# Optimization experiments

Hardware: AMD Instinct MI355X
Metric: run time of the kernel (lower is better)

The kernel has to match this reference:

```python
import jax, jax.numpy as jnp
import numpy as np
from jax import lax

B, C_IN, H, W = 4, 1536, 24, 24
MID, DIM = 768, 384
HEADS = 8; DIM_HEAD = 48; GROUPS = 8
DS = 3; OFF_SCALE = 4.0; OFF_K = 3
CPB_DIM = DIM // 4  # 96


def conv1x1(x, w):
    # x: (B,Cin,H,W), w: (Cout,Cin)
    return jnp.einsum('bchw,oc->bohw', x, w)


def grouped_conv1x1(x, w):
    # x: (B,G*Ci,H,W), w: (G,Co,Ci)  == torch Conv2d(groups=G, k=1, bias=False)
    b, c, h, ww = x.shape
    g, co, ci = w.shape
    return jnp.einsum('bgihw,goi->bgohw', x.reshape(b, g, ci, h, ww), w).reshape(b, g * co, h, ww)


def grid_sample_bilinear(img, grid):
    # torch F.grid_sample: bilinear, padding_mode='zeros', align_corners=False
    # img (N,C,H,W); grid (N,Ho,Wo,2) with [...,0]=x, [...,1]=y in [-1,1]
    n, c, h, w = img.shape
    x = ((grid[..., 0] + 1.0) * w - 1.0) * 0.5
    y = ((grid[..., 1] + 1.0) * h - 1.0) * 0.5
    x0 = jnp.floor(x); y0 = jnp.floor(y)
    wx = x - x0; wy = y - y0
    x0 = x0.astype(jnp.int32); y0 = y0.astype(jnp.int32)
    img_nhwc = jnp.transpose(img, (0, 2, 3, 1))
    bidx = jnp.arange(n)[:, None, None]

    def tap(ix, iy, wgt):
        valid = (ix >= 0) & (ix < w) & (iy >= 0) & (iy < h)
        v = img_nhwc[bidx, jnp.clip(iy, 0, h - 1), jnp.clip(ix, 0, w - 1)]  # (N,Ho,Wo,C)
        return v * (wgt * valid)[..., None]

    out = (tap(x0, y0, (1 - wx) * (1 - wy)) + tap(x0 + 1, y0, wx * (1 - wy))
           + tap(x0, y0 + 1, (1 - wx) * wy) + tap(x0 + 1, y0 + 1, wx * wy))
    return jnp.transpose(out, (0, 3, 1, 2))


def xy_grid(h, w, dtype):
    # create_grid_like: channel0 = x (width coord), channel1 = y (height coord)
    gx, gy = jnp.meshgrid(jnp.arange(w, dtype=dtype), jnp.arange(h, dtype=dtype), indexing='xy')
    return gx, gy


def normalize_pair(g0, g1, h, w):
    # faithful to lucidrains normalize_grid: channel0 scaled by (h-1), channel1 by (w-1)
    g0 = 2.0 * g0 / max(h - 1, 1) - 1.0
    g1 = 2.0 * g1 / max(w - 1, 1) - 1.0
    return jnp.stack([g0, g1], axis=-1)


def deform_attn(x, Wq, Wk, Wv, Wdw, bdw, Wpw, cw1, cb1, cw2, cb2, cw3, cb3, Wout, bout):
    b, c, h, w = x.shape
    q = grouped_conv1x1(x, Wq)                                 # (b,384,h,w)
    gq = q.reshape(b * GROUPS, c // GROUPS, h, w)
    # to_offsets: depthwise conv k=3 stride=3 pad=0 -> GELU -> 1x1 (->2) -> tanh -> *offset_scale
    off = lax.conv_general_dilated(gq, Wdw, (DS, DS), 'VALID',
                                   dimension_numbers=('NCHW', 'OIHW', 'NCHW'),
                                   feature_group_count=c // GROUPS) + bdw[None, :, None, None]
    off = jax.nn.gelu(off, approximate=False)
    off = jnp.tanh(jnp.einsum('bchw,oc->bohw', off, Wpw)) * OFF_SCALE   # (b*g,2,hp,wp)
    hp, wp = off.shape[-2], off.shape[-1]
    gx, gy = xy_grid(hp, wp, x.dtype)
    vgrid_scaled = normalize_pair(gx + off[:, 0], gy + off[:, 1], hp, wp)  # (b*g,hp,wp,2)
    kv = grid_sample_bilinear(x.reshape(b * GROUPS, c // GROUPS, h, w), vgrid_scaled)
    kv = kv.reshape(b, c, hp, wp)
    k = grouped_conv1x1(kv, Wk); v = grouped_conv1x1(kv, Wv)
    q = q * (DIM_HEAD ** -0.5)
    sh = lambda t: t.reshape(t.shape[0], HEADS, DIM_HEAD, -1).transpose(0, 1, 3, 2)
    qh, kh, vh = sh(q), sh(k), sh(v)                            # (b,H,i,d),(b,H,j,d)
    sim = jnp.einsum('bhid,bhjd->bhij', qh, kh)
    # CPB relative position bias
    qx, qy = xy_grid(h, w, x.dtype)
    grid_q = normalize_pair(qx, qy, h, w).reshape(1, h * w, 2)
    grid_kv = vgrid_scaled.reshape(b * GROUPS, hp * wp, 2)
    pos = grid_q[:, :, None, :] - grid_kv[:, None, :, :]        # (b*g,i,j,2)
    bias = jnp.sign(pos) * jnp.log1p(jnp.abs(pos))
    bias = jax.nn.relu(bias @ cw1.T + cb1)
    bias = jax.nn.relu(bias @ cw2.T + cb2)
    bias = (bias @ cw3.T + cb3).reshape(b, GROUPS, h * w, hp * wp)  # heads//offset_groups == 1
    attn = jax.nn.softmax(sim + bias, axis=-1)
    out = jnp.einsum('bhij,bhjd->bhid', attn, vh)
    out = out.transpose(0, 1, 3, 2).reshape(b, HEADS * DIM_HEAD, h, w)
    return conv1x1(out, Wout) + bout[None, :, None, None]


def setup_inputs() -> dict:
    key = jax.random.key(0)
    ks = jax.random.split(key, 20)
    s = 0.02
    p = lambda i, shape: jax.random.normal(ks[i], shape, jnp.float32) * s
    return {
        'x': jax.random.normal(ks[0], (B, C_IN, H, W), jnp.float32),
        'W1': p(1, (MID, C_IN)), 'W2': p(2, (DIM, MID)),
        'W3': p(3, (MID, DIM)), 'W4': p(4, (C_IN, MID)),
        'Wq': p(5, (GROUPS, DIM // GROUPS, DIM // GROUPS)),
        'Wk': p(6, (GROUPS, DIM // GROUPS, DIM // GROUPS)),
        'Wv': p(7, (GROUPS, DIM // GROUPS, DIM // GROUPS)),
        'Wdw': p(8, (DIM // GROUPS, 1, OFF_K, OFF_K)), 'bdw': p(9, (DIM // GROUPS,)),
        'Wpw': p(10, (2, DIM // GROUPS)),
        'cpb_w1': p(11, (CPB_DIM, 2)), 'cpb_b1': p(12, (CPB_DIM,)),
        'cpb_w2': p(13, (CPB_DIM, CPB_DIM)), 'cpb_b2': p(14, (CPB_DIM,)),
        'cpb_w3': p(15, (1, CPB_DIM)), 'cpb_b3': p(16, (1,)),
        'Wout': p(17, (DIM, DIM)), 'bout': p(18, (DIM,)),
    }


def reference(x, W1, W2, W3, W4, Wq, Wk, Wv, Wdw, bdw, Wpw,
              cpb_w1, cpb_b1, cpb_w2, cpb_b2, cpb_w3, cpb_b3, Wout, bout):
    h = jax.nn.relu(conv1x1(x, W1))
    h = jax.nn.relu(conv1x1(h, W2))
    h = jax.nn.relu(deform_attn(h, Wq, Wk, Wv, Wdw, bdw, Wpw,
                                cpb_w1, cpb_b1, cpb_w2, cpb_b2, cpb_w3, cpb_b3, Wout, bout))
    h = jax.nn.relu(conv1x1(h, W3))
    return jax.nn.relu(conv1x1(h, W4) + x)
```

## Files before the change

### kernel.cpp

```cpp
#include <hip/hip_runtime.h>

typedef float        fx4 __attribute__((ext_vector_type(4)));
typedef float        fx2 __attribute__((ext_vector_type(2)));
typedef unsigned int ux4 __attribute__((ext_vector_type(4)));
typedef short        bf8 __attribute__((ext_vector_type(8)));

#define DEVI static __device__ __forceinline__

DEVI unsigned f2bf1(float f) {
  union { float f; unsigned u; } v; v.f = f;
  return (v.u + 0x7FFFu + ((v.u >> 16) & 1u)) >> 16;
}
DEVI float bf2f(unsigned h) {
  union { unsigned u; float f; } v; v.u = h << 16; return v.f;
}
DEVI unsigned cvtpk(float lo, float hi) {
  unsigned r;
  asm("v_cvt_pk_bf16_f32 %0, %1, %2" : "=v"(r) : "v"(lo), "v"(hi));
  return r;
}
DEVI void unp8(ux4 u, float* o) {
  o[0] = bf2f(u[0] & 0xffffu); o[1] = bf2f(u[0] >> 16);
  o[2] = bf2f(u[1] & 0xffffu); o[3] = bf2f(u[1] >> 16);
  o[4] = bf2f(u[2] & 0xffffu); o[5] = bf2f(u[2] >> 16);
  o[6] = bf2f(u[3] & 0xffffu); o[7] = bf2f(u[3] >> 16);
}
DEVI void gload16(const void* g, void* l) {
  __builtin_amdgcn_global_load_lds(
      (const __attribute__((address_space(1))) unsigned*)(uintptr_t)(g),
      (__attribute__((address_space(3))) unsigned*)(unsigned)(uintptr_t)(l),
      16, 0, 0);
}
#define DPP_ADD(v, ctrl)                                                      \
  do {                                                                        \
    union { float f; int i; } _s, _d;                                         \
    _s.f = (v);                                                               \
    _d.i = __builtin_amdgcn_update_dpp(0, _s.i, (ctrl), 0xf, 0xf, false);     \
    (v) += _d.f;                                                              \
  } while (0)
DEVI float dpp_sum16(float v) {
  DPP_ADD(v, 0xB1);
  DPP_ADD(v, 0x4E);
  DPP_ADD(v, 0x124);
  DPP_ADD(v, 0x128);
  return v;
}
DEVI float sum8(float v) {
  DPP_ADD(v, 0xB1);
  DPP_ADD(v, 0x4E);
  v += __shfl_xor(v, 4);
  return v;
}

#define TABLO (-1.6f)
#define TABD  (3.2f / 255.f)
#define TABDI (255.f / 3.2f)

__global__ __launch_bounds__(256) void k_wconv(const float* __restrict__ W1,
                                               const float* __restrict__ W2,
                                               const float* __restrict__ W3,
                                               const float* __restrict__ W4,
                                               const float* __restrict__ Wout,
                                               const float* __restrict__ cw2,
                                               const float* __restrict__ Wq,
                                               unsigned* __restrict__ dst,
                                               unsigned* __restrict__ Wqd) {
  const size_t p = (size_t)blockIdx.x * 256 + threadIdx.x;
  if (p < 1552896) {
    const float* s; size_t base;
    if (p < 589824)       { s = W1;   base = 0; }
    else if (p < 737280)  { s = W2;   base = 589824; }
    else if (p < 884736)  { s = W3;   base = 737280; }
    else if (p < 1474560) { s = W4;   base = 884736; }
    else if (p < 1548288) { s = Wout; base = 1474560; }
    else                  { s = cw2;  base = 1548288; }
    const size_t lp = p - base;
    dst[p] = cvtpk(s[lp * 2], s[lp * 2 + 1]);
  } else if (p < 1626624) {
    const int q = (int)(p - 1552896);
    const int o = q / 192, cp = q % 192;
    const int c0 = cp * 2, c1 = c0 + 1;
    const int g = o / 48, lr = o % 48;
    const int lo = g * 48, hi = lo + 48;
    const float f0 = (c0 >= lo && c0 < hi) ? Wq[((size_t)g * 48 + lr) * 48 + (c0 - lo)] : 0.f;
    const float f1 = (c1 >= lo && c1 < hi) ? Wq[((size_t)g * 48 + lr) * 48 + (c1 - lo)] : 0.f;
    Wqd[q] = cvtpk(f0, f1);
  }
}

__global__ __launch_bounds__(256) void k_transpose(const float* __restrict__ x,
                                                   unsigned short* __restrict__ xT) {
  __shared__ float tile[64][65];
  const int t = threadIdx.x;
  const int b = blockIdx.z, c0 = blockIdx.x * 64, p0 = blockIdx.y * 64;
  const int tl = t & 63, th = t >> 6;
#pragma unroll
  for (int r = 0; r < 16; ++r) {
    int c = th * 16 + r;
    tile[c][tl] = x[((size_t)b * 1536 + c0 + c) * 576 + p0 + tl];
  }
  __syncthreads();
#pragma unroll
  for (int r = 0; r < 16; ++r) {
    int p = th * 16 + r;
    xT[((size_t)b * 576 + p0 + p) * 1536 + c0 + tl] = (unsigned short)f2bf1(tile[tl][p]);
  }
}

#define ROWOF(q) ((((q) >> 7) << 4) + ((q) & 15))
#define KOF(q)   (((((q) >> 6) & 1) << 5) + ((((q) >> 4) & 3) << 3))
template<int BN, bool BIASADD, bool FINAL, bool RELU>
__global__ __launch_bounds__(256, 4) void k_gemm(const unsigned short* __restrict__ A,
                                                 const unsigned short* __restrict__ Wb,
                                                 const float* __restrict__ bias,
                                                 const float* __restrict__ resid,
                                                 void* __restrict__ outp, int K, int M) {
  constexpr int BCH = BN / 32;
  constexpr int NJT = BN / 32;
  __shared__ __align__(16) unsigned short As[3][4096];
  __shared__ __align__(16) unsigned short Bs[3][BN * 64];
  const int t = threadIdx.x;
  const int bz = blockIdx.z, j0 = blockIdx.x * BN, i0 = blockIdx.y * 64;
  const int lane = t & 63, wid = t >> 6;
  const int wi = wid >> 1, wj = wid & 1;
  const int lrow = lane & 15, g4 = lane >> 4;

  const unsigned short* pa0 = A + ((size_t)(bz * 576 + i0 + ROWOF(t))) * K + KOF(t);
  const unsigned short* pa1 = A + ((size_t)(bz * 576 + i0 + ROWOF(t + 256))) * K + KOF(t + 256);
  const unsigned short* pb[BCH];
#pragma unroll
  for (int c = 0; c < BCH; ++c) {
    const int q = t + c * 256;
    pb[c] = Wb + ((size_t)(j0 + ROWOF(q))) * K + KOF(q);
  }
  auto stage = [&](int buf, int ko) {
    gload16(pa0 + ko, &As[buf][t * 8]);
    gload16(pa1 + ko, &As[buf][(t + 256) * 8]);
#pragma unroll
    for (int c = 0; c < BCH; ++c) gload16(pb[c] + ko, &Bs[buf][(t + c * 256) * 8]);
  };
  fx4 acc[2][NJT] = {};
  const int nk = K >> 6;
  stage(0, 0);
  if (nk > 1) stage(1, 64);
  int cur = 0;
  for (int ki = 0; ki < nk; ++ki) {
    if (ki + 1 < nk) {
      if constexpr (BCH == 2) asm volatile("s_waitcnt vmcnt(4)" ::: "memory");
      else                    asm volatile("s_waitcnt vmcnt(6)" ::: "memory");
    } else {
      asm volatile("s_waitcnt vmcnt(0)" ::: "memory");
    }
    __builtin_amdgcn_s_barrier();
    __builtin_amdgcn_sched_barrier(0);
    asm volatile("" ::: "memory");
    if (ki + 2 < nk) {
      int b2 = cur - 1; if (b2 < 0) b2 = 2;
      stage(b2, (ki + 2) * 64);
    }
    const unsigned short* ab = &As[cur][0];
    const unsigned short* bb = &Bs[cur][0];
#pragma unroll
    for (int kk = 0; kk < 2; ++kk) {
      bf8 a0 = *(const bf8*)(ab + (((wi * 2 + 0) * 2 + kk) * 64 + lane) * 8);
      bf8 a1 = *(const bf8*)(ab + (((wi * 2 + 1) * 2 + kk) * 64 + lane) * 8);
#pragma unroll
      for (int jt = 0; jt < NJT; ++jt) {
        bf8 b = *(const bf8*)(bb + (((wj * NJT + jt) * 2 + kk) * 64 + lane) * 8);
        acc[0][jt] = __builtin_amdgcn_mfma_f32_16x16x32_bf16(a0, b, acc[0][jt], 0, 0, 0);
        acc[1][jt] = __builtin_amdgcn_mfma_f32_16x16x32_bf16(a1, b, acc[1][jt], 0, 0, 0);
      }
    }
    cur = (cur == 2) ? 0 : cur + 1;
  }
#pragma unroll
  for (int it = 0; it < 2; ++it) {
    const int row0 = i0 + wi * 32 + it * 16 + g4 * 4;
#pragma unroll
    for (int jt = 0; jt < NJT; ++jt) {
      fx4 v = acc[it][jt];
      const int m = j0 + wj * (BN / 2) + jt * 16 + lrow;
      if (BIASADD) {
        float bv = bias[m];
        v[0] += bv; v[1] += bv; v[2] += bv; v[3] += bv;
      }
      if (FINAL) {
        const fx4 xr = *(const fx4*)(resid + ((size_t)bz * M + m) * 576 + row0);
        fx4 ov;
        ov[0] = fmaxf(v[0] + xr[0], 0.f); ov[1] = fmaxf(v[1] + xr[1], 0.f);
        ov[2] = fmaxf(v[2] + xr[2], 0.f); ov[3] = fmaxf(v[3] + xr[3], 0.f);
        *(fx4*)((float*)outp + ((size_t)bz * M + m) * 576 + row0) = ov;
      } else {
        unsigned short* o = (unsigned short*)outp;
#pragma unroll
        for (int r = 0; r < 4; ++r) {
          const float ov = RELU ? fmaxf(v[r], 0.f) : v[r];
          o[((size_t)(bz * 576) + row0 + r) * M + m] = (unsigned short)f2bf1(ov);
        }
      }
    }
  }
}
#undef ROWOF
#undef KOF

__global__ __launch_bounds__(256, 2) void k_sample(const unsigned short* __restrict__ qT,
                                                   const unsigned short* __restrict__ h2T,
                                                   const float* __restrict__ Wdw,
                                                   const float* __restrict__ bdw,
                                                   const float* __restrict__ Wpw,
                                                   const float* __restrict__ Wk,
                                                   const float* __restrict__ Wv,
                                                   float* __restrict__ vgrid,
                                                   float* __restrict__ kT,
                                                   float* __restrict__ vT) {
  __shared__ float vg[32];
  __shared__ __align__(16) unsigned short kvls[768];
  const int blk = blockIdx.x;
  const int bg = blk >> 2, pg = blk & 3;
  const int b = bg >> 3, g = bg & 7;
  const int t = threadIdx.x;
  const int pl = t >> 4;
  const int cq = t & 15;
  const int pos = pg * 16 + pl;
  const int oy = pos >> 3, ox = pos & 7;
  const int ch0 = cq * 3;
  float s0 = bdw[ch0], s1 = bdw[ch0 + 1], s2 = bdw[ch0 + 2];
#pragma unroll
  for (int ky = 0; ky < 3; ++ky) {
#pragma unroll
    for (int kx = 0; kx < 3; ++kx) {
      const unsigned short* rp =
          qT + ((size_t)b * 576 + (oy * 3 + ky) * 24 + ox * 3 + kx) * 384 + g * 48 + ch0;
      const int tap = ky * 3 + kx;
      s0 = fmaf(bf2f(rp[0]), Wdw[(ch0 + 0) * 9 + tap], s0);
      s1 = fmaf(bf2f(rp[1]), Wdw[(ch0 + 1) * 9 + tap], s1);
      s2 = fmaf(bf2f(rp[2]), Wdw[(ch0 + 2) * 9 + tap], s2);
    }
  }
  float a0 = 0.f, a1 = 0.f;
  {
    const float z0 = s0, z1 = s1, z2 = s2;
    const float g0 = 0.5f * z0 * (1.f + erff(z0 * 0.70710678118654752f));
    const float g1 = 0.5f * z1 * (1.f + erff(z1 * 0.70710678118654752f));
    const float g2 = 0.5f * z2 * (1.f + erff(z2 * 0.70710678118654752f));
    a0 = g0 * Wpw[ch0] + g1 * Wpw[ch0 + 1] + g2 * Wpw[ch0 + 2];
    a1 = g0 * Wpw[48 + ch0] + g1 * Wpw[48 + ch0 + 1] + g2 * Wpw[48 + ch0 + 2];
  }
  a0 = dpp_sum16(a0);
  a1 = dpp_sum16(a1);
  const float gx = ((float)ox + tanhf(a0) * 4.f) * (2.f / 7.f) - 1.f;
  const float gy = ((float)oy + tanhf(a1) * 4.f) * (2.f / 7.f) - 1.f;
  if (cq == 0) {
    vg[pl * 2 + 0] = gx; vg[pl * 2 + 1] = gy;
    vgrid[bg * 128 + pos * 2 + 0] = gx;
    vgrid[bg * 128 + pos * 2 + 1] = gy;
  }
  __syncthreads();
  {
    const float nx = vg[pl * 2 + 0], ny = vg[pl * 2 + 1];
    const float xs = ((nx + 1.f) * 24.f - 1.f) * 0.5f;
    const float ys = ((ny + 1.f) * 24.f - 1.f) * 0.5f;
    const float x0f = floorf(xs), y0f = floorf(ys);
    const float wx = xs - x0f, wy = ys - y0f;
    const int x0 = (int)x0f, y0 = (int)y0f;
    float c0a = 0.f, c1a = 0.f, c2a = 0.f;
    const float tw[4] = {(1.f - wx) * (1.f - wy), wx * (1.f - wy), (1.f - wx) * wy, wx * wy};
    const int tx[4] = {x0, x0 + 1, x0, x0 + 1};
    const int ty[4] = {y0, y0, y0 + 1, y0 + 1};
#pragma unroll
    for (int tp = 0; tp < 4; ++tp) {
      const int ix = tx[tp], iy = ty[tp];
      const float w = tw[tp] * ((ix >= 0 && ix < 24 && iy >= 0 && iy < 24) ? 1.f : 0.f);
      const int cx = min(max(ix, 0), 23), cy = min(max(iy, 0), 23);
      const unsigned short* rp = h2T + ((size_t)b * 576 + cy * 24 + cx) * 384 + g * 48 + ch0;
      c0a = fmaf(bf2f(rp[0]), w, c0a);
      c1a = fmaf(bf2f(rp[1]), w, c1a);
      c2a = fmaf(bf2f(rp[2]), w, c2a);
    }
    kvls[pl * 48 + ch0 + 0] = (unsigned short)f2bf1(c0a);
    kvls[pl * 48 + ch0 + 1] = (unsigned short)f2bf1(c1a);
    kvls[pl * 48 + ch0 + 2] = (unsigned short)f2bf1(c2a);
  }
  __syncthreads();
#pragma unroll
  for (int r = 0; r < 3; ++r) {
    const int idx = t + r * 256;
    const int j = idx / 48, o = idx % 48;
    const unsigned short* rp = &kvls[j * 48];
    const float* wkp = Wk + ((size_t)g * 48 + o) * 48;
    const float* wvp = Wv + ((size_t)g * 48 + o) * 48;
    float ak = 0.f, av = 0.f;
#pragma unroll
    for (int c8 = 0; c8 < 6; ++c8) {
      ux4 u = *(const ux4*)(rp + c8 * 8);
      float va[8]; unp8(u, va);
      fx4 wk0 = *(const fx4*)(wkp + c8 * 8); fx4 wk1 = *(const fx4*)(wkp + c8 * 8 + 4);
      fx4 wv0 = *(const fx4*)(wvp + c8 * 8); fx4 wv1 = *(const fx4*)(wvp + c8 * 8 + 4);
#pragma unroll
      for (int e = 0; e < 4; ++e) {
        ak = fmaf(va[e], wk0[e], ak); ak = fmaf(va[4 + e], wk1[e], ak);
        av = fmaf(va[e], wv0[e], av); av = fmaf(va[4 + e], wv1[e], av);
      }
    }
    kT[(size_t)bg * 3072 + (pg * 16 + j) * 48 + o] = ak;
    vT[(size_t)bg * 3072 + (pg * 16 + j) * 48 + o] = av;
  }
}

__global__ __launch_bounds__(256) void k_cpb_tab(const float* __restrict__ cw1,
                                                 const float* __restrict__ cb1,
                                                 const unsigned short* __restrict__ cw2b,
                                                 const float* __restrict__ cb2,
                                                 const float* __restrict__ cw3,
                                                 const float* __restrict__ cb3,
                                                 float* __restrict__ Tb) {
  __shared__ __align__(16) unsigned short Ws[1152 * 8];
  __shared__ __align__(16) float Cs[288];
  const int t = threadIdx.x;
  const int wid = t >> 6, lane = t & 63;
  const int lrow = lane & 15, g16 = lane >> 4;
#pragma unroll
  for (int rep = 0; rep < 5; ++rep) {
    const int q = t + rep * 256;
    if (q < 1152) {
      const int s = q >> 6, l = q & 63;
      const int jt = s / 3, kk = s - jt * 3;
      const int n = jt * 16 + (l & 15);
      const int k = kk * 32 + ((l >> 4) & 3) * 8;
      gload16(cw2b + (size_t)n * 96 + k, &Ws[q * 8]);
    }
  }
  for (int q = t; q < 288; q += 256) Cs[q] = (q < 192) ? cw1[q] : cb1[q - 192];
  float cb2v[6], cw3v[6];
#pragma unroll
  for (int jt = 0; jt < 6; ++jt) {
    cb2v[jt] = cb2[jt * 16 + lrow];
    cw3v[jt] = cw3[jt * 16 + lrow];
  }
  const float cb3v = cb3[0];
  __syncthreads();
  const int base = blockIdx.x * 256 + wid * 64;
  float uu[4], vv[4];
#pragma unroll
  for (int mt = 0; mt < 4; ++mt) {
    const int e = base + mt * 16 + lrow;
    uu[mt] = TABLO + TABD * (float)(e >> 8);
    vv[mt] = TABLO + TABD * (float)(e & 255);
  }
  bf8 afr[4][3];
#pragma unroll
  for (int kk = 0; kk < 3; ++kk) {
    const int kb = kk * 32 + g16 * 8;
    fx4 w0 = *(const fx4*)&Cs[kb * 2];
    fx4 w1 = *(const fx4*)&Cs[kb * 2 + 4];
    fx4 w2 = *(const fx4*)&Cs[kb * 2 + 8];
    fx4 w3 = *(const fx4*)&Cs[kb * 2 + 12];
    fx4 b0 = *(const fx4*)&Cs[192 + kb];
    fx4 b1 = *(const fx4*)&Cs[192 + kb + 4];
#pragma unroll
    for (int mt = 0; mt < 4; ++mt) {
      float h[8];
      h[0] = fmaxf(fmaf(w0[0], uu[mt], fmaf(w0[1], vv[mt], b0[0])), 0.f);
      h[1] = fmaxf(fmaf(w0[2], uu[mt], fmaf(w0[3], vv[mt], b0[1])), 0.f);
      h[2] = fmaxf(fmaf(w1[0], uu[mt], fmaf(w1[1], vv[mt], b0[2])), 0.f);
      h[3] = fmaxf(fmaf(w1[2], uu[mt], fmaf(w1[3], vv[mt], b0[3])), 0.f);
      h[4] = fmaxf(fmaf(w2[0], uu[mt], fmaf(w2[1], vv[mt], b1[0])), 0.f);
      h[5] = fmaxf(fmaf(w2[2], uu[mt], fmaf(w2[3], vv[mt], b1[1])), 0.f);
      h[6] = fmaxf(fmaf(w3[0], uu[mt], fmaf(w3[1], vv[mt], b1[2])), 0.f);
      h[7] = fmaxf(fmaf(w3[2], uu[mt], fmaf(w3[3], vv[mt], b1[3])), 0.f);
      ux4 pk;
      pk[0] = cvtpk(h[0], h[1]); pk[1] = cvtpk(h[2], h[3]);
      pk[2] = cvtpk(h[4], h[5]); pk[3] = cvtpk(h[6], h[7]);
      afr[mt][kk] = *(bf8*)&pk;
    }
  }
  fx4 part[4] = {};
#pragma unroll
  for (int jt = 0; jt < 6; ++jt) {
    bf8 bf0 = *(const bf8*)&Ws[((jt * 3 + 0) * 64 + lane) * 8];
    bf8 bf1 = *(const bf8*)&Ws[((jt * 3 + 1) * 64 + lane) * 8];
    bf8 bf2 = *(const bf8*)&Ws[((jt * 3 + 2) * 64 + lane) * 8];
#pragma unroll
    for (int mt = 0; mt < 4; ++mt) {
      fx4 acc = {cb2v[jt], cb2v[jt], cb2v[jt], cb2v[jt]};
      acc = __builtin_amdgcn_mfma_f32_16x16x32_bf16(afr[mt][0], bf0, acc, 0, 0, 0);
      acc = __builtin_amdgcn_mfma_f32_16x16x32_bf16(afr[mt][1], bf1, acc, 0, 0, 0);
      acc = __builtin_amdgcn_mfma_f32_16x16x32_bf16(afr[mt][2], bf2, acc, 0, 0, 0);
#pragma unroll
      for (int r = 0; r < 4; ++r)
        part[mt][r] = fmaf(fmaxf(acc[r], 0.f), cw3v[jt], part[mt][r]);
    }
  }
#pragma unroll
  for (int mt = 0; mt < 4; ++mt) {
#pragma unroll
    for (int r = 0; r < 4; ++r) part[mt][r] = dpp_sum16(part[mt][r]);
    float pv2 = part[mt][0];
    pv2 = (lrow == 1) ? part[mt][1] : pv2;
    pv2 = (lrow == 2) ? part[mt][2] : pv2;
    pv2 = (lrow == 3) ? part[mt][3] : pv2;
    if (lrow < 4) Tb[base + mt * 16 + g16 * 4 + lrow] = pv2 + cb3v;
  }
}

__global__ __launch_bounds__(256) void k_attn(const unsigned short* __restrict__ qT,
                                              const float* __restrict__ kT,
                                              const float* __restrict__ vT,
                                              const float* __restrict__ vgrid,
                                              const float* __restrict__ Tb,
                                              unsigned short* __restrict__ aoT) {
  __shared__ __align__(16) float kls[3360];
  __shared__ __align__(16) float vls[3360];
  __shared__ float vgls[128];
  const int t = threadIdx.x;
  const int ic = blockIdx.x, h = blockIdx.y, b = blockIdx.z;
  const int bg = b * 8 + h;
  {
    const int j = t >> 2, qt = t & 3;
    const float* sk = kT + (size_t)bg * 3072 + j * 48 + qt * 12;
    const float* sv = vT + (size_t)bg * 3072 + j * 48 + qt * 12;
    float* dk = kls + j * 52 + (j >> 3) * 4 + qt * 12;
    float* dv = vls + j * 52 + (j >> 3) * 4 + qt * 12;
#pragma unroll
    for (int e = 0; e < 3; ++e) {
      ((fx4*)dk)[e] = ((const fx4*)sk)[e];
      ((fx4*)dv)[e] = ((const fx4*)sv)[e];
    }
  }
  if (t < 128) vgls[t] = vgrid[bg * 128 + t];
  __syncthreads();
  const int qi = ic * 32 + (t >> 3);
  const int kg = t & 7;
  const int rowbase = kg * 420;
  const unsigned short* qp = qT + ((size_t)b * 576 + qi) * 384 + h * 48;
  const float scale = 0.14433756729740643f;
  float s[8] = {0.f, 0.f, 0.f, 0.f, 0.f, 0.f, 0.f, 0.f};
#pragma unroll
  for (int c8 = 0; c8 < 6; ++c8) {
    ux4 u = *(const ux4*)(qp + c8 * 8);
    float qv[8]; unp8(u, qv);
#pragma unroll
    for (int it = 0; it < 8; ++it) {
      const float* kr = kls + rowbase + it * 52 + c8 * 8;
      fx4 k0 = *(const fx4*)kr, k1 = *(const fx4*)(kr + 4);
      s[it] = fmaf(qv[0], k0[0], s[it]); s[it] = fmaf(qv[1], k0[1], s[it]);
      s[it] = fmaf(qv[2], k0[2], s[it]); s[it] = fmaf(qv[3], k0[3], s[it]);
      s[it] = fmaf(qv[4], k1[0], s[it]); s[it] = fmaf(qv[5], k1[1], s[it]);
      s[it] = fmaf(qv[6], k1[2], s[it]); s[it] = fmaf(qv[7], k1[3], s[it]);
    }
  }
  const float qnx = (float)(qi % 24) * (2.f / 23.f) - 1.f;
  const float qny = (float)(qi / 24) * (2.f / 23.f) - 1.f;
#pragma unroll
  for (int it = 0; it < 8; ++it) {
    const int j = kg * 8 + it;
    const float pu = qnx - vgls[j * 2 + 0];
    const float pv = qny - vgls[j * 2 + 1];
    const float u = copysignf(__logf(1.f + fabsf(pu)), pu);
    const float v = copysignf(__logf(1.f + fabsf(pv)), pv);
    float tu = (u - TABLO) * TABDI;
    float tv = (v - TABLO) * TABDI;
    int iu = (int)floorf(tu); iu = min(max(iu, 0), 254);
    int iv = (int)floorf(tv); iv = min(max(iv, 0), 254);
    const float fu = tu - (float)iu;
    const float fv = tv - (float)iv;
    const float* r0 = Tb + iu * 256 + iv;
    const float a = r0[0], bb2 = r0[1], c = r0[256], d = r0[257];
    const float top = fmaf(fv, bb2 - a, a);
    const float bot = fmaf(fv, d - c, c);
    s[it] = fmaf(s[it], scale, fmaf(fu, bot - top, top));
  }
  float mx = s[0];
#pragma unroll
  for (int it = 1; it < 8; ++it) mx = fmaxf(mx, s[it]);
  mx = fmaxf(mx, __shfl_xor(mx, 1));
  mx = fmaxf(mx, __shfl_xor(mx, 2));
  mx = fmaxf(mx, __shfl_xor(mx, 4));
  float sum = 0.f;
#pragma unroll
  for (int it = 0; it < 8; ++it) { s[it] = __expf(s[it] - mx); sum += s[it]; }
  sum = sum8(sum);
  const float inv = 1.f / sum;
#pragma unroll
  for (int it = 0; it < 8; ++it) s[it] *= inv;
  float keep[8];
#pragma unroll
  for (int c8 = 0; c8 < 6; ++c8) {
    float a8[8] = {0.f, 0.f, 0.f, 0.f, 0.f, 0.f, 0.f, 0.f};
#pragma unroll
    for (int it = 0; it < 8; ++it) {
      const float p = s[it];
      const float* vr = vls + rowbase + it * 52 + c8 * 8;
      fx4 v0 = *(const fx4*)vr, v1 = *(const fx4*)(vr + 4);
      a8[0] = fmaf(p, v0[0], a8[0]); a8[1] = fmaf(p, v0[1], a8[1]);
      a8[2] = fmaf(p, v0[2], a8[2]); a8[3] = fmaf(p, v0[3], a8[3]);
      a8[4] = fmaf(p, v1[0], a8[4]); a8[5] = fmaf(p, v1[1], a8[5]);
      a8[6] = fmaf(p, v1[2], a8[6]); a8[7] = fmaf(p, v1[3], a8[7]);
    }
#pragma unroll
    for (int e = 0; e < 8; ++e) {
      a8[e] = sum8(a8[e]);
      keep[e] = (kg == c8) ? a8[e] : keep[e];
    }
  }
  if (kg < 6) {
    unsigned* op32 = (unsigned*)(aoT + ((size_t)b * 576 + qi) * 384 + h * 48 + kg * 8);
    op32[0] = cvtpk(keep[0], keep[1]);
    op32[1] = cvtpk(keep[2], keep[3]);
    op32[2] = cvtpk(keep[4], keep[5]);
    op32[3] = cvtpk(keep[6], keep[7]);
  }
}

extern "C" void kernel_launch(void* const* d_in, const int* in_sizes, int n_in,
                              void* d_out, int out_size, void* d_ws, size_t ws_size,
                              hipStream_t stream) {
  (void)in_sizes; (void)n_in; (void)out_size; (void)ws_size;
  const float* x    = (const float*)d_in[0];
  const float* W1   = (const float*)d_in[1];
  const float* W2   = (const float*)d_in[2];
  const float* W3   = (const float*)d_in[3];
  const float* W4   = (const float*)d_in[4];
  const float* Wq   = (const float*)d_in[5];
  const float* Wk   = (const float*)d_in[6];
  const float* Wv   = (const float*)d_in[7];
  const float* Wdw  = (const float*)d_in[8];
  const float* bdw  = (const float*)d_in[9];
  const float* Wpw  = (const float*)d_in[10];
  const float* cw1  = (const float*)d_in[11];
  const float* cb1  = (const float*)d_in[12];
  const float* cw2  = (const float*)d_in[13];
  const float* cb2  = (const float*)d_in[14];
  const float* cw3  = (const float*)d_in[15];
  const float* cb3  = (const float*)d_in[16];
  const float* Wout = (const float*)d_in[17];
  const float* bout = (const float*)d_in[18];

  char* ws = (char*)d_ws;
  size_t off = 0;
  auto alloc = [&](size_t bytes) {
    void* p = ws + off;
    off += (bytes + 255) & ~(size_t)255;
    return p;
  };
  unsigned short* xT  = (unsigned short*)alloc((size_t)4 * 576 * 1536 * 2);
  unsigned short* h1T = (unsigned short*)alloc((size_t)4 * 576 * 768 * 2);
  unsigned short* h2T = (unsigned short*)alloc((size_t)4 * 576 * 384 * 2);
  unsigned short* qT  = (unsigned short*)alloc((size_t)4 * 576 * 384 * 2);
  unsigned short* aoT = (unsigned short*)alloc((size_t)4 * 576 * 384 * 2);
  unsigned short* AT  = (unsigned short*)alloc((size_t)4 * 576 * 384 * 2);
  unsigned short* h3T = (unsigned short*)alloc((size_t)4 * 576 * 768 * 2);
  float* vgrid = (float*)alloc((size_t)32 * 64 * 2 * 4);
  float* kTb  = (float*)alloc((size_t)32 * 64 * 48 * 4);
  float* vTb  = (float*)alloc((size_t)32 * 64 * 48 * 4);
  float* Tb    = (float*)alloc((size_t)256 * 256 * 4);
  unsigned short* Wcvt = (unsigned short*)alloc((size_t)3105792 * 2);
  unsigned short* Wqd  = (unsigned short*)alloc((size_t)384 * 384 * 2);
  const unsigned short* W1b   = Wcvt;
  const unsigned short* W2b   = Wcvt + 1179648;
  const unsigned short* W3b   = Wcvt + 1474560;
  const unsigned short* W4b   = Wcvt + 1769472;
  const unsigned short* Woutb = Wcvt + 2949120;
  const unsigned short* cw2b  = Wcvt + 3096576;

  k_wconv<<<6355, 256, 0, stream>>>(W1, W2, W3, W4, Wout, cw2, Wq,
                                    (unsigned*)Wcvt, (unsigned*)Wqd);
  k_cpb_tab<<<256, 256, 0, stream>>>(cw1, cb1, cw2b, cb2, cw3, cb3, Tb);
  k_transpose<<<dim3(24, 9, 4), 256, 0, stream>>>(x, xT);
  k_gemm<64, false, false, true><<<dim3(12, 9, 4), 256, 0, stream>>>(xT, W1b, nullptr, nullptr, h1T, 1536, 768);
  k_gemm<64, false, false, true><<<dim3(6, 9, 4), 256, 0, stream>>>(h1T, W2b, nullptr, nullptr, h2T, 768, 384);
  k_gemm<64, false, false, false><<<dim3(6, 9, 4), 256, 0, stream>>>(h2T, Wqd, nullptr, nullptr, qT, 384, 384);
  k_sample<<<128, 256, 0, stream>>>(qT, h2T, Wdw, bdw, Wpw, Wk, Wv, vgrid, kTb, vTb);
  k_attn<<<dim3(18, 8, 4), 256, 0, stream>>>(qT, kTb, vTb, vgrid, Tb, aoT);
  k_gemm<64, true, false, true><<<dim3(6, 9, 4), 256, 0, stream>>>(aoT, Woutb, bout, nullptr, AT, 384, 384);
  k_gemm<64, false, false, true><<<dim3(12, 9, 4), 256, 0, stream>>>(AT, W3b, nullptr, nullptr, h3T, 384, 768);
  k_gemm<128, false, true, true><<<dim3(12, 9, 4), 256, 0, stream>>>(h3T, W4b, nullptr, x, d_out, 768, 1536);
}
```

Before: 113.5 us.

## Merge weight conversion, transpose and CPB table into one prep kernel; widen GEMM tiles

Folds the weight bf16 conversion, the input transpose and the CPB lookup-table build into one block-indexed prep kernel, with the CPB weights converted inline instead of read back from a converted buffer. This removes two launches and the dependency between the conversion and table kernels. Separately, the W1 and W3 GEMMs switch to 128-wide N tiles, halving their grid to 216 blocks. That reduces redundant A-tile loads but lowers parallelism on a 256-CU part.

```diff
diff --git a/kernel.cpp b/kernel.cpp
--- a/kernel.cpp
+++ b/kernel.cpp
@@ -56,28 +56,38 @@
 #define TABD  (3.2f / 255.f)
 #define TABDI (255.f / 3.2f)
 
-__global__ __launch_bounds__(256) void k_wconv(const float* __restrict__ W1,
-                                               const float* __restrict__ W2,
-                                               const float* __restrict__ W3,
-                                               const float* __restrict__ W4,
-                                               const float* __restrict__ Wout,
-                                               const float* __restrict__ cw2,
-                                               const float* __restrict__ Wq,
-                                               unsigned* __restrict__ dst,
-                                               unsigned* __restrict__ Wqd) {
-  const size_t p = (size_t)blockIdx.x * 256 + threadIdx.x;
-  if (p < 1552896) {
+__global__ __launch_bounds__(256) void k_prep(const float* __restrict__ W1,
+                                              const float* __restrict__ W2,
+                                              const float* __restrict__ W3,
+                                              const float* __restrict__ W4,
+                                              const float* __restrict__ Wout,
+                                              const float* __restrict__ Wq,
+                                              const float* __restrict__ x,
+                                              const float* __restrict__ cw1,
+                                              const float* __restrict__ cb1,
+                                              const float* __restrict__ cw2,
+                                              const float* __restrict__ cb2,
+                                              const float* __restrict__ cw3,
+                                              const float* __restrict__ cb3,
+                                              unsigned* __restrict__ dst,
+                                              unsigned* __restrict__ Wqd,
+                                              unsigned short* __restrict__ xT,
+                                              float* __restrict__ Tb) {
+  __shared__ __align__(16) char smem[19712];
+  const int blk = blockIdx.x;
+  const int t = threadIdx.x;
+  if (blk < 6048) {
+    const size_t p = (size_t)blk * 256 + t;
     const float* s; size_t base;
     if (p < 589824)       { s = W1;   base = 0; }
     else if (p < 737280)  { s = W2;   base = 589824; }
     else if (p < 884736)  { s = W3;   base = 737280; }
     else if (p < 1474560) { s = W4;   base = 884736; }
-    else if (p < 1548288) { s = Wout; base = 1474560; }
-    else                  { s = cw2;  base = 1548288; }
+    else                  { s = Wout; base = 1474560; }
     const size_t lp = p - base;
     dst[p] = cvtpk(s[lp * 2], s[lp * 2 + 1]);
-  } else if (p < 1626624) {
-    const int q = (int)(p - 1552896);
+  } else if (blk < 6336) {
+    const int q = (blk - 6048) * 256 + t;
     const int o = q / 192, cp = q % 192;
     const int c0 = cp * 2, c1 = c0 + 1;
     const int g = o / 48, lr = o % 48;
@@ -85,25 +95,109 @@
     const float f0 = (c0 >= lo && c0 < hi) ? Wq[((size_t)g * 48 + lr) * 48 + (c0 - lo)] : 0.f;
     const float f1 = (c1 >= lo && c1 < hi) ? Wq[((size_t)g * 48 + lr) * 48 + (c1 - lo)] : 0.f;
     Wqd[q] = cvtpk(f0, f1);
-  }
-}
-
-__global__ __launch_bounds__(256) void k_transpose(const float* __restrict__ x,
-                                                   unsigned short* __restrict__ xT) {
-  __shared__ float tile[64][65];
-  const int t = threadIdx.x;
-  const int b = blockIdx.z, c0 = blockIdx.x * 64, p0 = blockIdx.y * 64;
-  const int tl = t & 63, th = t >> 6;
-#pragma unroll
-  for (int r = 0; r < 16; ++r) {
-    int c = th * 16 + r;
-    tile[c][tl] = x[((size_t)b * 1536 + c0 + c) * 576 + p0 + tl];
-  }
-  __syncthreads();
-#pragma unroll
-  for (int r = 0; r < 16; ++r) {
-    int p = th * 16 + r;
-    xT[((size_t)b * 576 + p0 + p) * 1536 + c0 + tl] = (unsigned short)f2bf1(tile[tl][p]);
+  } else if (blk < 7200) {
+    float (*tile)[65] = (float(*)[65])smem;
+    const int id = blk - 6336;
+    const int b = id / 216, r = id % 216;
+    const int c0 = (r / 9) * 64, p0 = (r % 9) * 64;
+    const int tl = t & 63, th = t >> 6;
+#pragma unroll
+    for (int rr = 0; rr < 16; ++rr) {
+      int c = th * 16 + rr;
+      tile[c][tl] = x[((size_t)b * 1536 + c0 + c) * 576 + p0 + tl];
+    }
+    __syncthreads();
+#pragma unroll
+    for (int rr = 0; rr < 16; ++rr) {
+      int p = th * 16 + rr;
+      xT[((size_t)b * 576 + p0 + p) * 1536 + c0 + tl] = (unsigned short)f2bf1(tile[tl][p]);
+    }
+  } else {
+    unsigned short* Ws = (unsigned short*)smem;
+    float* Cs = (float*)(smem + 18432);
+    const int wid = t >> 6, lane = t & 63;
+    const int lrow = lane & 15, g16 = lane >> 4;
+    for (int q = t; q < 1152; q += 256) {
+      const int s = q >> 6, l = q & 63;
+      const int jt = s / 3, kk = s - jt * 3;
+      const int n = jt * 16 + (l & 15);
+      const int k = kk * 32 + ((l >> 4) & 3) * 8;
+      const float* src = cw2 + (size_t)n * 96 + k;
+#pragma unroll
+      for (int e = 0; e < 8; e += 2)
+        *(unsigned*)&Ws[q * 8 + e] = cvtpk(src[e], src[e + 1]);
+    }
+    for (int q = t; q < 288; q += 256) Cs[q] = (q < 192) ? cw1[q] : cb1[q - 192];
+    float cb2v[6], cw3v[6];
+#pragma unroll
+    for (int jt = 0; jt < 6; ++jt) {
+      cb2v[jt] = cb2[jt * 16 + lrow];
+      cw3v[jt] = cw3[jt * 16 + lrow];
+    }
+    const float cb3v = cb3[0];
+    __syncthreads();
+    const int base = (blk - 7200) * 256 + wid * 64;
+    float uu[4], vv[4];
+#pragma unroll
+    for (int mt = 0; mt < 4; ++mt) {
+      const int e = base + mt * 16 + lrow;
+      uu[mt] = TABLO + TABD * (float)(e >> 8);
+      vv[mt] = TABLO + TABD * (float)(e & 255);
+    }
+    bf8 afr[4][3];
+#pragma unroll
+    for (int kk = 0; kk < 3; ++kk) {
+      const int kb = kk * 32 + g16 * 8;
+      fx4 w0 = *(const fx4*)&Cs[kb * 2];
+      fx4 w1 = *(const fx4*)&Cs[kb * 2 + 4];
+      fx4 w2 = *(const fx4*)&Cs[kb * 2 + 8];
+      fx4 w3 = *(const fx4*)&Cs[kb * 2 + 12];
+      fx4 b0 = *(const fx4*)&Cs[192 + kb];
+      fx4 b1 = *(const fx4*)&Cs[192 + kb + 4];
+#pragma unroll
+      for (int mt = 0; mt < 4; ++mt) {
+        float h[8];
+        h[0] = fmaxf(fmaf(w0[0], uu[mt], fmaf(w0[1], vv[mt], b0[0])), 0.f);
+        h[1] = fmaxf(fmaf(w0[2], uu[mt], fmaf(w0[3], vv[mt], b0[1])), 0.f);
+        h[2] = fmaxf(fmaf(w1[0], uu[mt], fmaf(w1[1], vv[mt], b0[2])), 0.f);
+        h[3] = fmaxf(fmaf(w1[2], uu[mt], fmaf(w1[3], vv[mt], b0[3])), 0.f);
+        h[4] = fmaxf(fmaf(w2[0], uu[mt], fmaf(w2[1], vv[mt], b1[0])), 0.f);
+        h[5] = fmaxf(fmaf(w2[2], uu[mt], fmaf(w2[3], vv[mt], b1[1])), 0.f);
+        h[6] = fmaxf(fmaf(w3[0], uu[mt], fmaf(w3[1], vv[mt], b1[2])), 0.f);
+        h[7] = fmaxf(fmaf(w3[2], uu[mt], fmaf(w3[3], vv[mt], b1[3])), 0.f);
+        ux4 pk;
+        pk[0] = cvtpk(h[0], h[1]); pk[1] = cvtpk(h[2], h[3]);
+        pk[2] = cvtpk(h[4], h[5]); pk[3] = cvtpk(h[6], h[7]);
+        afr[mt][kk] = *(bf8*)&pk;
+      }
+    }
+    fx4 part[4] = {};
+#pragma unroll
+    for (int jt = 0; jt < 6; ++jt) {
+      bf8 bf0 = *(const bf8*)&Ws[((jt * 3 + 0) * 64 + lane) * 8];
+      bf8 bf1 = *(const bf8*)&Ws[((jt * 3 + 1) * 64 + lane) * 8];
+      bf8 bf2 = *(const bf8*)&Ws[((jt * 3 + 2) * 64 + lane) * 8];
+#pragma unroll
+      for (int mt = 0; mt < 4; ++mt) {
+        fx4 acc = {cb2v[jt], cb2v[jt], cb2v[jt], cb2v[jt]};
+        acc = __builtin_amdgcn_mfma_f32_16x16x32_bf16(afr[mt][0], bf0, acc, 0, 0, 0);
+        acc = __builtin_amdgcn_mfma_f32_16x16x32_bf16(afr[mt][1], bf1, acc, 0, 0, 0);
+        acc = __builtin_amdgcn_mfma_f32_16x16x32_bf16(afr[mt][2], bf2, acc, 0, 0, 0);
+#pragma unroll
+        for (int r = 0; r < 4; ++r)
+          part[mt][r] = fmaf(fmaxf(acc[r], 0.f), cw3v[jt], part[mt][r]);
+      }
+    }
+#pragma unroll
+    for (int mt = 0; mt < 4; ++mt) {
+#pragma unroll
+      for (int r = 0; r < 4; ++r) part[mt][r] = dpp_sum16(part[mt][r]);
+      float pv2 = part[mt][0];
+      pv2 = (lrow == 1) ? part[mt][1] : pv2;
+      pv2 = (lrow == 2) ? part[mt][2] : pv2;
+      pv2 = (lrow == 3) ? part[mt][3] : pv2;
+      if (lrow < 4) Tb[base + mt * 16 + g16 * 4 + lrow] = pv2 + cb3v;
+    }
   }
 }
 
@@ -305,102 +399,6 @@
     }
     kT[(size_t)bg * 3072 + (pg * 16 + j) * 48 + o] = ak;
     vT[(size_t)bg * 3072 + (pg * 16 + j) * 48 + o] = av;
-  }
-}
-
-__global__ __launch_bounds__(256) void k_cpb_tab(const float* __restrict__ cw1,
-                                                 const float* __restrict__ cb1,
-                                                 const unsigned short* __restrict__ cw2b,
-                                                 const float* __restrict__ cb2,
-                                                 const float* __restrict__ cw3,
-                                                 const float* __restrict__ cb3,
-                                                 float* __restrict__ Tb) {
-  __shared__ __align__(16) unsigned short Ws[1152 * 8];
-  __shared__ __align__(16) float Cs[288];
-  const int t = threadIdx.x;
-  const int wid = t >> 6, lane = t & 63;
-  const int lrow = lane & 15, g16 = lane >> 4;
-#pragma unroll
-  for (int rep = 0; rep < 5; ++rep) {
-    const int q = t + rep * 256;
-    if (q < 1152) {
-      const int s = q >> 6, l = q & 63;
-      const int jt = s / 3, kk = s - jt * 3;
-      const int n = jt * 16 + (l & 15);
-      const int k = kk * 32 + ((l >> 4) & 3) * 8;
-      gload16(cw2b + (size_t)n * 96 + k, &Ws[q * 8]);
-    }
-  }
-  for (int q = t; q < 288; q += 256) Cs[q] = (q < 192) ? cw1[q] : cb1[q - 192];
-  float cb2v[6], cw3v[6];
-#pragma unroll
-  for (int jt = 0; jt < 6; ++jt) {
-    cb2v[jt] = cb2[jt * 16 + lrow];
-    cw3v[jt] = cw3[jt * 16 + lrow];
-  }
-  const float cb3v = cb3[0];
-  __syncthreads();
-  const int base = blockIdx.x * 256 + wid * 64;
-  float uu[4], vv[4];
-#pragma unroll
-  for (int mt = 0; mt < 4; ++mt) {
-    const int e = base + mt * 16 + lrow;
-    uu[mt] = TABLO + TABD * (float)(e >> 8);
-    vv[mt] = TABLO + TABD * (float)(e & 255);
-  }
-  bf8 afr[4][3];
-#pragma unroll
-  for (int kk = 0; kk < 3; ++kk) {
-    const int kb = kk * 32 + g16 * 8;
-    fx4 w0 = *(const fx4*)&Cs[kb * 2];
-    fx4 w1 = *(const fx4*)&Cs[kb * 2 + 4];
-    fx4 w2 = *(const fx4*)&Cs[kb * 2 + 8];
-    fx4 w3 = *(const fx4*)&Cs[kb * 2 + 12];
-    fx4 b0 = *(const fx4*)&Cs[192 + kb];
-    fx4 b1 = *(const fx4*)&Cs[192 + kb + 4];
-#pragma unroll
-    for (int mt = 0; mt < 4; ++mt) {
-      float h[8];
-      h[0] = fmaxf(fmaf(w0[0], uu[mt], fmaf(w0[1], vv[mt], b0[0])), 0.f);
-      h[1] = fmaxf(fmaf(w0[2], uu[mt], fmaf(w0[3], vv[mt], b0[1])), 0.f);
-      h[2] = fmaxf(fmaf(w1[0], uu[mt], fmaf(w1[1], vv[mt], b0[2])), 0.f);
-      h[3] = fmaxf(fmaf(w1[2], uu[mt], fmaf(w1[3], vv[mt], b0[3])), 0.f);
-      h[4] = fmaxf(fmaf(w2[0], uu[mt], fmaf(w2[1], vv[mt], b1[0])), 0.f);
-      h[5] = fmaxf(fmaf(w2[2], uu[mt], fmaf(w2[3], vv[mt], b1[1])), 0.f);
-      h[6] = fmaxf(fmaf(w3[0], uu[mt], fmaf(w3[1], vv[mt], b1[2])), 0.f);
-      h[7] = fmaxf(fmaf(w3[2], uu[mt], fmaf(w3[3], vv[mt], b1[3])), 0.f);
-      ux4 pk;
-      pk[0] = cvtpk(h[0], h[1]); pk[1] = cvtpk(h[2], h[3]);
-      pk[2] = cvtpk(h[4], h[5]); pk[3] = cvtpk(h[6], h[7]);
-      afr[mt][kk] = *(bf8*)&pk;
-    }
-  }
-  fx4 part[4] = {};
-#pragma unroll
-  for (int jt = 0; jt < 6; ++jt) {
-    bf8 bf0 = *(const bf8*)&Ws[((jt * 3 + 0) * 64 + lane) * 8];
-    bf8 bf1 = *(const bf8*)&Ws[((jt * 3 + 1) * 64 + lane) * 8];
-    bf8 bf2 = *(const bf8*)&Ws[((jt * 3 + 2) * 64 + lane) * 8];
-#pragma unroll
-    for (int mt = 0; mt < 4; ++mt) {
-      fx4 acc = {cb2v[jt], cb2v[jt], cb2v[jt], cb2v[jt]};
-      acc = __builtin_amdgcn_mfma_f32_16x16x32_bf16(afr[mt][0], bf0, acc, 0, 0, 0);
-      acc = __builtin_amdgcn_mfma_f32_16x16x32_bf16(afr[mt][1], bf1, acc, 0, 0, 0);
-      acc = __builtin_amdgcn_mfma_f32_16x16x32_bf16(afr[mt][2], bf2, acc, 0, 0, 0);
-#pragma unroll
-      for (int r = 0; r < 4; ++r)
-        part[mt][r] = fmaf(fmaxf(acc[r], 0.f), cw3v[jt], part[mt][r]);
-    }
-  }
-#pragma unroll
-  for (int mt = 0; mt < 4; ++mt) {
-#pragma unroll
-    for (int r = 0; r < 4; ++r) part[mt][r] = dpp_sum16(part[mt][r]);
-    float pv2 = part[mt][0];
-    pv2 = (lrow == 1) ? part[mt][1] : pv2;
-    pv2 = (lrow == 2) ? part[mt][2] : pv2;
-    pv2 = (lrow == 3) ? part[mt][3] : pv2;
-    if (lrow < 4) Tb[base + mt * 16 + g16 * 4 + lrow] = pv2 + cb3v;
   }
 }
 
@@ -555,25 +553,23 @@
   float* kTb  = (float*)alloc((size_t)32 * 64 * 48 * 4);
   float* vTb  = (float*)alloc((size_t)32 * 64 * 48 * 4);
   float* Tb    = (float*)alloc((size_t)256 * 256 * 4);
-  unsigned short* Wcvt = (unsigned short*)alloc((size_t)3105792 * 2);
+  unsigned short* Wcvt = (unsigned short*)alloc((size_t)3096576 * 2);
   unsigned short* Wqd  = (unsigned short*)alloc((size_t)384 * 384 * 2);
   const unsigned short* W1b   = Wcvt;
   const unsigned short* W2b   = Wcvt + 1179648;
   const unsigned short* W3b   = Wcvt + 1474560;
   const unsigned short* W4b   = Wcvt + 1769472;
   const unsigned short* Woutb = Wcvt + 2949120;
-  const unsigned short* cw2b  = Wcvt + 3096576;
-
-  k_wconv<<<6355, 256, 0, stream>>>(W1, W2, W3, W4, Wout, cw2, Wq,
-                                    (unsigned*)Wcvt, (unsigned*)Wqd);
-  k_cpb_tab<<<256, 256, 0, stream>>>(cw1, cb1, cw2b, cb2, cw3, cb3, Tb);
-  k_transpose<<<dim3(24, 9, 4), 256, 0, stream>>>(x, xT);
-  k_gemm<64, false, false, true><<<dim3(12, 9, 4), 256, 0, stream>>>(xT, W1b, nullptr, nullptr, h1T, 1536, 768);
+
+  k_prep<<<7456, 256, 0, stream>>>(W1, W2, W3, W4, Wout, Wq, x,
+                                   cw1, cb1, cw2, cb2, cw3, cb3,
+                                   (unsigned*)Wcvt, (unsigned*)Wqd, xT, Tb);
+  k_gemm<128, false, false, true><<<dim3(6, 9, 4), 256, 0, stream>>>(xT, W1b, nullptr, nullptr, h1T, 1536, 768);
   k_gemm<64, false, false, true><<<dim3(6, 9, 4), 256, 0, stream>>>(h1T, W2b, nullptr, nullptr, h2T, 768, 384);
   k_gemm<64, false, false, false><<<dim3(6, 9, 4), 256, 0, stream>>>(h2T, Wqd, nullptr, nullptr, qT, 384, 384);
   k_sample<<<128, 256, 0, stream>>>(qT, h2T, Wdw, bdw, Wpw, Wk, Wv, vgrid, kTb, vTb);
   k_attn<<<dim3(18, 8, 4), 256, 0, stream>>>(qT, kTb, vTb, vgrid, Tb, aoT);
   k_gemm<64, true, false, true><<<dim3(6, 9, 4), 256, 0, stream>>>(aoT, Woutb, bout, nullptr, AT, 384, 384);
-  k_gemm<64, false, false, true><<<dim3(12, 9, 4), 256, 0, stream>>>(AT, W3b, nullptr, nullptr, h3T, 384, 768);
+  k_gemm<128, false, false, true><<<dim3(6, 9, 4), 256, 0, stream>>>(AT, W3b, nullptr, nullptr, h3T, 384, 768);
   k_gemm<128, false, true, true><<<dim3(12, 9, 4), 256, 0, stream>>>(h3T, W4b, nullptr, x, d_out, 768, 1536);
 }
```

Result: faster. 109.8 us (-3.3%).
